# Performance work log

Hardware: AMD Instinct MI355X
Metric: run time of the kernel (lower is better)

Reference implementation:

```python
import jax, jax.numpy as jnp
import numpy as np

NUM_QUBITS = 21
NUM_LAYERS = 4
ACTION_DIM = 18
STATE_DIM = 2 ** NUM_QUBITS  # amplitude register size


def _rx(t):
    c = jnp.cos(t / 2)
    s = jnp.sin(t / 2)
    return jnp.stack([jnp.stack([c + 0j, -1j * s]), jnp.stack([-1j * s, c + 0j])]).astype(jnp.complex64)


def _ry(t):
    c = jnp.cos(t / 2)
    s = jnp.sin(t / 2)
    return jnp.stack([jnp.stack([c, -s]), jnp.stack([s, c])]).astype(jnp.complex64)


def _rz(t):
    e = jnp.exp(-1j * t / 2).astype(jnp.complex64)
    z = jnp.zeros_like(e)
    return jnp.stack([jnp.stack([e, z]), jnp.stack([z, jnp.conj(e)])])


def apply_1q(psi, U, q):
    # wire 0 is the most-significant bit (PennyLane convention)
    s = psi.reshape(2 ** q, 2, -1)
    s = jnp.einsum('ab,xbz->xaz', U, s)
    return s.reshape(-1)


def apply_cnot(psi, c, t):
    a, b = (c, t) if c < t else (t, c)
    s = psi.reshape(2 ** a, 2, 2 ** (b - a - 1), 2, -1)
    ctrl_ax = 1 if c < t else 3
    tgt_ax = 3 if c < t else 1
    s0 = jax.lax.index_in_dim(s, 0, axis=ctrl_ax, keepdims=False)
    s1 = jax.lax.index_in_dim(s, 1, axis=ctrl_ax, keepdims=False)
    tgt_in_slab = tgt_ax if tgt_ax < ctrl_ax else tgt_ax - 1
    s1 = jnp.flip(s1, axis=tgt_in_slab)  # X on target where control==1
    s = jnp.stack([s0, s1], axis=ctrl_ax)
    return s.reshape(-1)


def _layer(psi, lp, entangle):
    # lp: (NUM_QUBITS, 3) rotation angles for this layer
    for q in range(NUM_QUBITS):
        psi = apply_1q(psi, _rx(lp[q, 0]), q)
        psi = apply_1q(psi, _ry(lp[q, 1]), q)
        psi = apply_1q(psi, _rz(lp[q, 2]), q)
    if entangle:
        for q in range(NUM_QUBITS - 1):
            psi = apply_cnot(psi, q, q + 1)
        psi = apply_cnot(psi, NUM_QUBITS - 1, 0)
    return psi


def setup_inputs() -> dict:
    key = jax.random.key(0)
    k1, k2, k3, k4 = jax.random.split(key, 4)
    state = jax.random.normal(k1, (STATE_DIM,), dtype=jnp.float32)
    circuit_params = jax.random.normal(k2, (NUM_LAYERS * NUM_QUBITS * 3,), dtype=jnp.float32) * 0.01
    bound = 1.0 / np.sqrt(NUM_QUBITS)
    head_w = jax.random.uniform(k3, (ACTION_DIM, NUM_QUBITS), jnp.float32, -bound, bound)
    head_b = jax.random.uniform(k4, (ACTION_DIM,), jnp.float32, -bound, bound)
    return {'state': state, 'circuit_params': circuit_params, 'head_w': head_w, 'head_b': head_b}


def reference(state, circuit_params, head_w, head_b):
    # Amplitude encoding: normalize (state_dim == 2**num_qubits so no padding needed)
    norm = jnp.linalg.norm(state)
    inv = jnp.where(norm > 0, 1.0 / jnp.maximum(norm, 1e-30), 0.0)
    basis0 = jnp.zeros((STATE_DIM,), jnp.float32).at[0].set(1.0)
    amp = jnp.where(norm > 0, state * inv, basis0)
    psi = amp.astype(jnp.complex64)

    lp = circuit_params.reshape(NUM_LAYERS, NUM_QUBITS, 3)
    for layer in range(NUM_LAYERS):
        psi = _layer(psi, lp[layer], layer < NUM_LAYERS - 1)

    # Pauli-Z expectation values per qubit from |psi|^2
    probs = psi.real ** 2 + psi.imag ** 2
    zvals = []
    for q in range(NUM_QUBITS):
        p = probs.reshape(2 ** q, 2, -1)
        zvals.append(p[:, 0, :].sum() - p[:, 1, :].sum())
    meas = jnp.stack(zvals).astype(jnp.float32)

    logits = head_w @ meas + head_b
    return jax.nn.softmax(logits, axis=-1)
```

## Files before the change

### kernel.cpp

```cpp
#include <hip/hip_runtime.h>

#define NQ 21
#define DIM (1 << NQ)
#define NL 4
#define ADIM 18

__device__ __forceinline__ float2 cmul(float2 a, float2 b) {
    return make_float2(a.x * b.x - a.y * b.y, a.x * b.y + a.y * b.x);
}
__device__ __forceinline__ float2 cfma2(float2 u0, float2 a, float2 u1, float2 b) {
    return make_float2(u0.x * a.x - u0.y * a.y + u1.x * b.x - u1.y * b.y,
                       u0.x * a.y + u0.y * a.x + u1.x * b.y + u1.y * b.x);
}

__device__ __forceinline__ int pxor8(int x) {
    x ^= x >> 1; x ^= x >> 2; x ^= x >> 4;
    return x & 0xFF;
}

__global__ void k_mats(const float* __restrict__ p, float2* __restrict__ mats) {
    int g = blockIdx.x * blockDim.x + threadIdx.x;
    if (g >= NL * NQ) return;
    const float* ang = p + g * 3;
    float a = ang[0], b = ang[1], c = ang[2];
    float ca = cosf(0.5f * a), sa = sinf(0.5f * a);
    float cb = cosf(0.5f * b), sb = sinf(0.5f * b);
    float cc = cosf(0.5f * c), sc = sinf(0.5f * c);
    float2 m00 = make_float2(cb * ca,  sb * sa);
    float2 m01 = make_float2(-sb * ca, -cb * sa);
    float2 m10 = make_float2(sb * ca,  -cb * sa);
    float2 m11 = make_float2(cb * ca,  -sb * sa);
    float2 ph0 = make_float2(cc, -sc);
    float2 ph1 = make_float2(cc,  sc);
    mats[g * 4 + 0] = cmul(ph0, m00);
    mats[g * 4 + 1] = cmul(ph0, m01);
    mats[g * 4 + 2] = cmul(ph1, m10);
    mats[g * 4 + 3] = cmul(ph1, m11);
}

__global__ __launch_bounds__(512) void k_passA(float2* __restrict__ psi, const float2* __restrict__ mats,
                                               int layer, int entangle, float* __restrict__ partials) {
    __shared__ float4 lds4[4096];
    float2* lds = (float2*)lds4;
    const int blk = blockIdx.x, tid = threadIdx.x;

    const float4* g4 = (const float4*)psi + blk * 4096;
    for (int i = tid; i < 4096; i += 512) lds4[i] = g4[i];
    __syncthreads();

    for (int k = 0; k < 13; ++k) {
        const float2* U = mats + (layer * NQ + (20 - k)) * 4;
        float2 u00 = U[0], u01 = U[1], u10 = U[2], u11 = U[3];
        int m = 1 << k;
        for (int p = tid; p < 4096; p += 512) {
            int i0 = ((p >> k) << (k + 1)) | (p & (m - 1));
            int i1 = i0 | m;
            float2 a = lds[i0], b = lds[i1];
            lds[i0] = cfma2(u00, a, u01, b);
            lds[i1] = cfma2(u10, a, u11, b);
        }
        __syncthreads();
    }

    if (partials) {
        float tot = 0.f;
        float ones[NQ];
#pragma unroll
        for (int q = 0; q < NQ; ++q) ones[q] = 0.f;
        for (int t = tid; t < 8192; t += 512) {
            float2 a = lds[t];
            float pr = a.x * a.x + a.y * a.y;
            int gidx = (blk << 13) | t;
            tot += pr;
#pragma unroll
            for (int q = 0; q < NQ; ++q)
                ones[q] += ((gidx >> (20 - q)) & 1) ? pr : 0.f;
        }
        for (int off = 32; off; off >>= 1) {
            tot += __shfl_down(tot, off, 64);
#pragma unroll
            for (int q = 0; q < NQ; ++q) ones[q] += __shfl_down(ones[q], off, 64);
        }
        __syncthreads();
        float* red = (float*)lds4;
        int wave = tid >> 6, lane = tid & 63;
        if (lane == 0) {
            red[wave * 22 + 21] = tot;
#pragma unroll
            for (int q = 0; q < NQ; ++q) red[wave * 22 + q] = ones[q];
        }
        __syncthreads();
        if (tid < 22) {
            float s = 0.f;
            for (int w = 0; w < 8; ++w) s += red[w * 22 + tid];
            partials[blk * 22 + tid] = s;
        }
    } else if (entangle) {
        float4* o4 = (float4*)psi + blk * 4096;
        int cbit = (blk & 1) << 12;
        for (int t = tid; t < 4096; t += 512) {
            int j0 = 2 * t, j1 = j0 + 1;
            int s0 = (j0 ^ ((j0 >> 1) & 0xFFF)) ^ cbit;
            int s1 = (j1 ^ ((j1 >> 1) & 0xFFF)) ^ cbit;
            float2 e0 = lds[s0], e1 = lds[s1];
            o4[t] = make_float4(e0.x, e0.y, e1.x, e1.y);
        }
    } else {
        float4* o4 = (float4*)psi + blk * 4096;
        for (int t = tid; t < 4096; t += 512) o4[t] = lds4[t];
    }
}

__global__ __launch_bounds__(512) void k_passB(const float* __restrict__ state, float2* __restrict__ psi,
                                               const float2* __restrict__ mats, int layer, int c4, int c1) {
    __shared__ float2 lds[8192];
    const int blk = blockIdx.x, tid = threadIdx.x;

    if (state) {
        const float4* s4 = (const float4*)state;
        for (int t = tid; t < 2048; t += 512) {
            int hs = t >> 3, c = t & 7;
            float4 v = s4[(hs << 11) | (blk << 3) | c];
            int base = hs * 32 + 4 * c;
            lds[base + 0] = make_float2(v.x, 0.f);
            lds[base + 1] = make_float2(v.y, 0.f);
            lds[base + 2] = make_float2(v.z, 0.f);
            lds[base + 3] = make_float2(v.w, 0.f);
        }
    } else {
        const float4* p4 = (const float4*)psi;
        for (int t = tid; t < 4096; t += 512) {
            int hs = t >> 4, c = t & 15;
            float4 v = p4[(hs << 12) | (blk << 4) | c];
            int hodd = c4 ? (hs ^ 128) : hs;
            lds[hs * 32 + 2 * c]       = make_float2(v.x, v.y);
            lds[hodd * 32 + 2 * c + 1] = make_float2(v.z, v.w);
        }
    }
    __syncthreads();

    for (int kb = 0; kb < 8; ++kb) {
        const float2* U = mats + (layer * NQ + (7 - kb)) * 4;
        float2 u00 = U[0], u01 = U[1], u10 = U[2], u11 = U[3];
        for (int p = tid; p < 4096; p += 512) {
            int l = p & 31, hp = p >> 5;
            int h0 = ((hp >> kb) << (kb + 1)) | (hp & ((1 << kb) - 1));
            int i0 = h0 * 32 + l;
            int i1 = i0 + (32 << kb);
            float2 a = lds[i0], b = lds[i1];
            lds[i0] = cfma2(u00, a, u01, b);
            lds[i1] = cfma2(u10, a, u11, b);
        }
        __syncthreads();
    }

    float4* o4 = (float4*)psi;
    for (int t = tid; t < 4096; t += 512) {
        int hs = t >> 4, c = t & 15;
        int hd = c1 ? pxor8(hs) : hs;
        float2 e0 = lds[hs * 32 + 2 * c], e1 = lds[hs * 32 + 2 * c + 1];
        o4[(hd << 12) | (blk << 4) | c] = make_float4(e0.x, e0.y, e1.x, e1.y);
    }
}

__global__ void k_final(const float* __restrict__ partials, const float* __restrict__ head_w,
                        const float* __restrict__ head_b, float* __restrict__ out) {
    __shared__ float red[22];
    __shared__ float meas[NQ];
    __shared__ float lg[ADIM];
    int tid = threadIdx.x;
    if (tid < 22) {
        float s = 0.f;
        for (int b = 0; b < 256; ++b) s += partials[b * 22 + tid];
        red[tid] = s;
    }
    __syncthreads();
    if (tid < NQ) {
        float tot = red[21];
        meas[tid] = (tot > 0.f) ? (1.f - 2.f * red[tid] / tot) : 1.f;
    }
    __syncthreads();
    if (tid < ADIM) {
        float s = head_b[tid];
        for (int q = 0; q < NQ; ++q) s += head_w[tid * NQ + q] * meas[q];
        lg[tid] = s;
    }
    __syncthreads();
    if (tid == 0) {
        float m = lg[0];
        for (int a = 1; a < ADIM; ++a) m = fmaxf(m, lg[a]);
        float s = 0.f;
        for (int a = 0; a < ADIM; ++a) s += expf(lg[a] - m);
        float inv = 1.f / s;
        for (int a = 0; a < ADIM; ++a) out[a] = expf(lg[a] - m) * inv;
    }
}

extern "C" void kernel_launch(void* const* d_in, const int* in_sizes, int n_in,
                              void* d_out, int out_size, void* d_ws, size_t ws_size,
                              hipStream_t stream) {
    const float* state   = (const float*)d_in[0];
    const float* cparams = (const float*)d_in[1];
    const float* head_w  = (const float*)d_in[2];
    const float* head_b  = (const float*)d_in[3];
    float* out = (float*)d_out;

    char* ws = (char*)d_ws;
    float2* psi      = (float2*)ws;
    float2* mats     = (float2*)(ws + (size_t)DIM * 8);
    float*  partials = (float*)(ws + (size_t)DIM * 8 + 4096);

    k_mats<<<1, 128, 0, stream>>>(cparams, mats);
    k_passB<<<256, 512, 0, stream>>>(state,   psi, mats, 0, 0, 1);
    k_passA<<<256, 512, 0, stream>>>(psi, mats, 0, 1, nullptr);
    k_passB<<<256, 512, 0, stream>>>(nullptr, psi, mats, 1, 1, 1);
    k_passA<<<256, 512, 0, stream>>>(psi, mats, 1, 1, nullptr);
    k_passB<<<256, 512, 0, stream>>>(nullptr, psi, mats, 2, 1, 1);
    k_passA<<<256, 512, 0, stream>>>(psi, mats, 2, 1, nullptr);
    k_passB<<<256, 512, 0, stream>>>(nullptr, psi, mats, 3, 1, 0);
    k_passA<<<256, 512, 0, stream>>>(psi, mats, 3, 0, partials);

    k_final<<<1, 64, 0, stream>>>(partials, head_w, head_b, out);
}
```

Baseline: 233.9 us.

## Fuse all circuit passes into one persistent kernel with grid-wide barriers

Replaces the ten separate kernel launches (matrix setup, alternating pass A/B per layer, final reduction) with a single persistent kernel of 512 blocks. Blocks synchronise through an atomic-counter grid barrier, and gate matrices are computed per block in shared memory. The tiles are smaller (4096 amplitudes), and some gates are applied in registers right after the global loads. The aim is to remove launch gaps and tail effects between passes. In exchange it relies on all 512 blocks being co-resident, adds spin-wait barrier overhead, and needs a memset per call.

```diff
diff --git a/kernel.cpp b/kernel.cpp
--- a/kernel.cpp
+++ b/kernel.cpp
@@ -4,195 +4,252 @@
 #define DIM (1 << NQ)
 #define NL 4
 #define ADIM 18
-
-__device__ __forceinline__ float2 cmul(float2 a, float2 b) {
-    return make_float2(a.x * b.x - a.y * b.y, a.x * b.y + a.y * b.x);
-}
+#define GB 512
+#define NT 512
+
 __device__ __forceinline__ float2 cfma2(float2 u0, float2 a, float2 u1, float2 b) {
     return make_float2(u0.x * a.x - u0.y * a.y + u1.x * b.x - u1.y * b.y,
                        u0.x * a.y + u0.y * a.x + u1.x * b.y + u1.y * b.x);
 }
 
-__device__ __forceinline__ int pxor8(int x) {
-    x ^= x >> 1; x ^= x >> 2; x ^= x >> 4;
-    return x & 0xFF;
-}
-
-__global__ void k_mats(const float* __restrict__ p, float2* __restrict__ mats) {
-    int g = blockIdx.x * blockDim.x + threadIdx.x;
-    if (g >= NL * NQ) return;
-    const float* ang = p + g * 3;
-    float a = ang[0], b = ang[1], c = ang[2];
-    float ca = cosf(0.5f * a), sa = sinf(0.5f * a);
-    float cb = cosf(0.5f * b), sb = sinf(0.5f * b);
-    float cc = cosf(0.5f * c), sc = sinf(0.5f * c);
-    float2 m00 = make_float2(cb * ca,  sb * sa);
-    float2 m01 = make_float2(-sb * ca, -cb * sa);
-    float2 m10 = make_float2(sb * ca,  -cb * sa);
-    float2 m11 = make_float2(cb * ca,  -sb * sa);
-    float2 ph0 = make_float2(cc, -sc);
-    float2 ph1 = make_float2(cc,  sc);
-    mats[g * 4 + 0] = cmul(ph0, m00);
-    mats[g * 4 + 1] = cmul(ph0, m01);
-    mats[g * 4 + 2] = cmul(ph1, m10);
-    mats[g * 4 + 3] = cmul(ph1, m11);
-}
-
-__global__ __launch_bounds__(512) void k_passA(float2* __restrict__ psi, const float2* __restrict__ mats,
-                                               int layer, int entangle, float* __restrict__ partials) {
-    __shared__ float4 lds4[4096];
-    float2* lds = (float2*)lds4;
-    const int blk = blockIdx.x, tid = threadIdx.x;
-
-    const float4* g4 = (const float4*)psi + blk * 4096;
-    for (int i = tid; i < 4096; i += 512) lds4[i] = g4[i];
+struct GateU { float2 u00, u01, u10, u11; };
+
+__device__ __forceinline__ void bfly(float2& a, float2& b, const GateU& U) {
+    float2 na = cfma2(U.u00, a, U.u01, b);
+    float2 nb = cfma2(U.u10, a, U.u11, b);
+    a = na; b = nb;
+}
+
+__device__ __forceinline__ void gbar(int* bar, int phase) {
     __syncthreads();
-
-    for (int k = 0; k < 13; ++k) {
-        const float2* U = mats + (layer * NQ + (20 - k)) * 4;
-        float2 u00 = U[0], u01 = U[1], u10 = U[2], u11 = U[3];
-        int m = 1 << k;
-        for (int p = tid; p < 4096; p += 512) {
-            int i0 = ((p >> k) << (k + 1)) | (p & (m - 1));
-            int i1 = i0 | m;
-            float2 a = lds[i0], b = lds[i1];
-            lds[i0] = cfma2(u00, a, u01, b);
-            lds[i1] = cfma2(u10, a, u11, b);
-        }
-        __syncthreads();
-    }
-
-    if (partials) {
-        float tot = 0.f;
-        float ones[NQ];
-#pragma unroll
-        for (int q = 0; q < NQ; ++q) ones[q] = 0.f;
-        for (int t = tid; t < 8192; t += 512) {
-            float2 a = lds[t];
-            float pr = a.x * a.x + a.y * a.y;
-            int gidx = (blk << 13) | t;
-            tot += pr;
-#pragma unroll
-            for (int q = 0; q < NQ; ++q)
-                ones[q] += ((gidx >> (20 - q)) & 1) ? pr : 0.f;
-        }
-        for (int off = 32; off; off >>= 1) {
-            tot += __shfl_down(tot, off, 64);
-#pragma unroll
-            for (int q = 0; q < NQ; ++q) ones[q] += __shfl_down(ones[q], off, 64);
-        }
-        __syncthreads();
-        float* red = (float*)lds4;
-        int wave = tid >> 6, lane = tid & 63;
-        if (lane == 0) {
-            red[wave * 22 + 21] = tot;
-#pragma unroll
-            for (int q = 0; q < NQ; ++q) red[wave * 22 + q] = ones[q];
-        }
-        __syncthreads();
-        if (tid < 22) {
-            float s = 0.f;
-            for (int w = 0; w < 8; ++w) s += red[w * 22 + tid];
-            partials[blk * 22 + tid] = s;
-        }
-    } else if (entangle) {
-        float4* o4 = (float4*)psi + blk * 4096;
-        int cbit = (blk & 1) << 12;
-        for (int t = tid; t < 4096; t += 512) {
-            int j0 = 2 * t, j1 = j0 + 1;
-            int s0 = (j0 ^ ((j0 >> 1) & 0xFFF)) ^ cbit;
-            int s1 = (j1 ^ ((j1 >> 1) & 0xFFF)) ^ cbit;
-            float2 e0 = lds[s0], e1 = lds[s1];
-            o4[t] = make_float4(e0.x, e0.y, e1.x, e1.y);
-        }
-    } else {
-        float4* o4 = (float4*)psi + blk * 4096;
-        for (int t = tid; t < 4096; t += 512) o4[t] = lds4[t];
-    }
-}
-
-__global__ __launch_bounds__(512) void k_passB(const float* __restrict__ state, float2* __restrict__ psi,
-                                               const float2* __restrict__ mats, int layer, int c4, int c1) {
-    __shared__ float2 lds[8192];
-    const int blk = blockIdx.x, tid = threadIdx.x;
-
-    if (state) {
-        const float4* s4 = (const float4*)state;
-        for (int t = tid; t < 2048; t += 512) {
-            int hs = t >> 3, c = t & 7;
-            float4 v = s4[(hs << 11) | (blk << 3) | c];
-            int base = hs * 32 + 4 * c;
-            lds[base + 0] = make_float2(v.x, 0.f);
-            lds[base + 1] = make_float2(v.y, 0.f);
-            lds[base + 2] = make_float2(v.z, 0.f);
-            lds[base + 3] = make_float2(v.w, 0.f);
-        }
-    } else {
-        const float4* p4 = (const float4*)psi;
-        for (int t = tid; t < 4096; t += 512) {
-            int hs = t >> 4, c = t & 15;
-            float4 v = p4[(hs << 12) | (blk << 4) | c];
-            int hodd = c4 ? (hs ^ 128) : hs;
-            lds[hs * 32 + 2 * c]       = make_float2(v.x, v.y);
-            lds[hodd * 32 + 2 * c + 1] = make_float2(v.z, v.w);
-        }
+    if (threadIdx.x == 0) {
+        __threadfence();
+        atomicAdd(bar, 1);
+        const int target = (phase + 1) * GB;
+        while (atomicAdd(bar, 0) < target) __builtin_amdgcn_s_sleep(4);
+        __threadfence();
     }
     __syncthreads();
-
-    for (int kb = 0; kb < 8; ++kb) {
-        const float2* U = mats + (layer * NQ + (7 - kb)) * 4;
-        float2 u00 = U[0], u01 = U[1], u10 = U[2], u11 = U[3];
-        for (int p = tid; p < 4096; p += 512) {
-            int l = p & 31, hp = p >> 5;
-            int h0 = ((hp >> kb) << (kb + 1)) | (hp & ((1 << kb) - 1));
-            int i0 = h0 * 32 + l;
-            int i1 = i0 + (32 << kb);
-            float2 a = lds[i0], b = lds[i1];
-            lds[i0] = cfma2(u00, a, u01, b);
-            lds[i1] = cfma2(u10, a, u11, b);
-        }
-        __syncthreads();
-    }
-
-    float4* o4 = (float4*)psi;
-    for (int t = tid; t < 4096; t += 512) {
-        int hs = t >> 4, c = t & 15;
-        int hd = c1 ? pxor8(hs) : hs;
-        float2 e0 = lds[hs * 32 + 2 * c], e1 = lds[hs * 32 + 2 * c + 1];
-        o4[(hd << 12) | (blk << 4) | c] = make_float4(e0.x, e0.y, e1.x, e1.y);
-    }
-}
-
-__global__ void k_final(const float* __restrict__ partials, const float* __restrict__ head_w,
-                        const float* __restrict__ head_b, float* __restrict__ out) {
-    __shared__ float red[22];
+}
+
+__global__ __launch_bounds__(NT, 4) void qpn_kernel(
+    const float* __restrict__ state, const float* __restrict__ cp,
+    const float* __restrict__ head_w, const float* __restrict__ head_b,
+    float* __restrict__ out, float2* __restrict__ psi, float* __restrict__ partials,
+    int* __restrict__ bar)
+{
+    __shared__ float2 tile[4096];
+    __shared__ GateU mats[NL * NQ];
     __shared__ float meas[NQ];
     __shared__ float lg[ADIM];
-    int tid = threadIdx.x;
-    if (tid < 22) {
-        float s = 0.f;
-        for (int b = 0; b < 256; ++b) s += partials[b * 22 + tid];
-        red[tid] = s;
+    const int tid = threadIdx.x;
+    const int blk = blockIdx.x;
+    float4* psi4 = (float4*)psi;
+    float4* t4 = (float4*)tile;
+    int phase = 0;
+
+    if (tid < NL * NQ) {
+        float a = cp[tid * 3 + 0], b = cp[tid * 3 + 1], c = cp[tid * 3 + 2];
+        float ca = cosf(0.5f * a), sa = sinf(0.5f * a);
+        float cb = cosf(0.5f * b), sb = sinf(0.5f * b);
+        float cc = cosf(0.5f * c), sc = sinf(0.5f * c);
+        float2 m00 = make_float2(cb * ca,  sb * sa);
+        float2 m01 = make_float2(-sb * ca, -cb * sa);
+        float2 m10 = make_float2(sb * ca,  -cb * sa);
+        float2 m11 = make_float2(cb * ca,  -sb * sa);
+        GateU U;
+        U.u00 = make_float2(cc * m00.x + sc * m00.y, cc * m00.y - sc * m00.x);
+        U.u01 = make_float2(cc * m01.x + sc * m01.y, cc * m01.y - sc * m01.x);
+        U.u10 = make_float2(cc * m10.x - sc * m10.y, cc * m10.y + sc * m10.x);
+        U.u11 = make_float2(cc * m11.x - sc * m11.y, cc * m11.y + sc * m11.x);
+        mats[tid] = U;
     }
     __syncthreads();
-    if (tid < NQ) {
-        float tot = red[21];
-        meas[tid] = (tot > 0.f) ? (1.f - 2.f * red[tid] / tot) : 1.f;
-    }
-    __syncthreads();
-    if (tid < ADIM) {
-        float s = head_b[tid];
-        for (int q = 0; q < NQ; ++q) s += head_w[tid * NQ + q] * meas[q];
-        lg[tid] = s;
-    }
-    __syncthreads();
-    if (tid == 0) {
-        float m = lg[0];
-        for (int a = 1; a < ADIM; ++a) m = fmaxf(m, lg[a]);
-        float s = 0.f;
-        for (int a = 0; a < ADIM; ++a) s += expf(lg[a] - m);
-        float inv = 1.f / s;
-        for (int a = 0; a < ADIM; ++a) out[a] = expf(lg[a] - m) * inv;
+
+    for (int layer = 0; layer < NL; ++layer) {
+        if (layer == 0) {
+            const float4* s4 = (const float4*)state;
+            for (int it = 0; it < 2; ++it) {
+                int f2 = it * NT + tid;
+                int h = f2 >> 1, c2 = f2 & 1;
+                float4 w = s4[(h << 10) | (blk << 1) | c2];
+                t4[h * 4 + 2 * c2]     = make_float4(w.x, 0.f, w.y, 0.f);
+                t4[h * 4 + 2 * c2 + 1] = make_float4(w.z, 0.f, w.w, 0.f);
+            }
+            __syncthreads();
+            for (int kb = 0; kb <= 8; ++kb) {
+                GateU U = mats[layer * NQ + (8 - kb)];
+                for (int it = 0; it < 4; ++it) {
+                    int p = it * NT + tid;
+                    int l = p & 7, hp = p >> 3;
+                    int h0 = ((hp >> kb) << (kb + 1)) | (hp & ((1 << kb) - 1));
+                    int i0 = h0 * 8 + l;
+                    bfly(tile[i0], tile[i0 + (8 << kb)], U);
+                }
+                __syncthreads();
+            }
+        } else {
+            float2 v[8];
+            float4 w[4];
+            for (int i = 0; i < 4; ++i) {
+                int f = i * NT + tid;
+                int h = f >> 2, c = f & 3;
+                w[i] = psi4[(h << 11) | (blk << 2) | c];
+            }
+#pragma unroll
+            for (int i = 0; i < 4; ++i) {
+                v[2 * i]     = make_float2(w[i].x, w[i].y);
+                v[2 * i + 1] = make_float2(w[i ^ 2].z, w[i ^ 2].w);
+            }
+            {
+                GateU U0 = mats[layer * NQ + 0];
+#pragma unroll
+                for (int s = 0; s < 8; ++s) if (!(s & 4)) bfly(v[s], v[s | 4], U0);
+                GateU U1 = mats[layer * NQ + 1];
+#pragma unroll
+                for (int s = 0; s < 8; ++s) if (!(s & 2)) bfly(v[s], v[s | 2], U1);
+            }
+            for (int i = 0; i < 4; ++i)
+                t4[i * NT + tid] = make_float4(v[2 * i].x, v[2 * i].y, v[2 * i + 1].x, v[2 * i + 1].y);
+            __syncthreads();
+            for (int kb = 0; kb <= 6; ++kb) {
+                GateU U = mats[layer * NQ + (8 - kb)];
+                for (int it = 0; it < 4; ++it) {
+                    int p = it * NT + tid;
+                    int l = p & 7, hp = p >> 3;
+                    int h0 = ((hp >> kb) << (kb + 1)) | (hp & ((1 << kb) - 1));
+                    int i0 = h0 * 8 + l;
+                    bfly(tile[i0], tile[i0 + (8 << kb)], U);
+                }
+                __syncthreads();
+            }
+        }
+        {
+            int srcmask = (layer < 3) ? 0xFF : 0;
+            for (int i = 0; i < 4; ++i) {
+                int f = i * NT + tid;
+                int h = f >> 2, c = f & 3;
+                int hs = h ^ ((h >> 1) & srcmask);
+                float2 e0 = tile[hs * 8 + 2 * c], e1 = tile[hs * 8 + 2 * c + 1];
+                psi4[(h << 11) | (blk << 2) | c] = make_float4(e0.x, e0.y, e1.x, e1.y);
+            }
+        }
+        gbar(bar, phase++);
+
+        {
+            const float4* ga = psi4 + (size_t)blk * 2048;
+            float2 v[8];
+            float4 w[4];
+            for (int i = 0; i < 4; ++i) w[i] = ga[i * NT + tid];
+#pragma unroll
+            for (int i = 0; i < 4; ++i) {
+                v[2 * i]     = make_float2(w[i].x, w[i].y);
+                v[2 * i + 1] = make_float2(w[i].z, w[i].w);
+            }
+            GateU U20 = mats[layer * NQ + 20];
+#pragma unroll
+            for (int s = 0; s < 8; s += 2) bfly(v[s], v[s + 1], U20);
+            GateU U10 = mats[layer * NQ + 10];
+#pragma unroll
+            for (int s = 0; s < 8; ++s) if (!(s & 2)) bfly(v[s], v[s | 2], U10);
+            GateU U9 = mats[layer * NQ + 9];
+#pragma unroll
+            for (int s = 0; s < 8; ++s) if (!(s & 4)) bfly(v[s], v[s | 4], U9);
+            for (int i = 0; i < 4; ++i)
+                t4[i * NT + tid] = make_float4(v[2 * i].x, v[2 * i].y, v[2 * i + 1].x, v[2 * i + 1].y);
+        }
+        __syncthreads();
+        for (int k = 1; k <= 9; ++k) {
+            GateU U = mats[layer * NQ + (20 - k)];
+            int m = 1 << k;
+            for (int it = 0; it < 4; ++it) {
+                int p = it * NT + tid;
+                int i0 = ((p >> k) << (k + 1)) | (p & (m - 1));
+                bfly(tile[i0], tile[i0 | m], U);
+            }
+            __syncthreads();
+        }
+        if (layer < 3) {
+            float4* oa = psi4 + (size_t)blk * 2048;
+            int cb = (blk & 1) << 11;
+            for (int i = 0; i < 4; ++i) {
+                int f = i * NT + tid;
+                int s0 = ((2 * f) ^ (f & 0x7FF)) ^ cb;
+                float2 e0 = tile[s0], e1 = tile[s0 ^ 1];
+                oa[f] = make_float4(e0.x, e0.y, e1.x, e1.y);
+            }
+            gbar(bar, phase++);
+        } else {
+            float tot = 0.f, ones[NQ];
+#pragma unroll
+            for (int q = 0; q < NQ; ++q) ones[q] = 0.f;
+            for (int it = 0; it < 8; ++it) {
+                int j = it * NT + tid;
+                float2 a2 = tile[j];
+                float pr = a2.x * a2.x + a2.y * a2.y;
+                int gidx = (blk << 12) | j;
+                tot += pr;
+#pragma unroll
+                for (int q = 0; q < NQ; ++q)
+                    ones[q] += pr * (float)((gidx >> (20 - q)) & 1);
+            }
+            for (int off = 32; off; off >>= 1) {
+                tot += __shfl_down(tot, off, 64);
+#pragma unroll
+                for (int q = 0; q < NQ; ++q) ones[q] += __shfl_down(ones[q], off, 64);
+            }
+            __syncthreads();
+            float* red = (float*)tile;
+            int wv = tid >> 6, ln = tid & 63;
+            if (ln == 0) {
+                red[wv * 22 + 21] = tot;
+#pragma unroll
+                for (int q = 0; q < NQ; ++q) red[wv * 22 + q] = ones[q];
+            }
+            __syncthreads();
+            if (tid < 22) {
+                float s = 0.f;
+                for (int wvi = 0; wvi < 8; ++wvi) s += red[wvi * 22 + tid];
+                partials[blk * 22 + tid] = s;
+            }
+            gbar(bar, phase++);
+        }
+    }
+
+    if (blk == 0) {
+        float* red = (float*)tile;
+        int col = tid % 22, grp = tid / 22;
+        if (tid < 506) {
+            float s = 0.f;
+            for (int r = grp; r < GB; r += 23) s += partials[r * 22 + col];
+            red[grp * 22 + col] = s;
+        }
+        __syncthreads();
+        if (tid < 22) {
+            float t2 = 0.f;
+            for (int g = 0; g < 23; ++g) t2 += red[g * 22 + tid];
+            red[600 + tid] = t2;
+        }
+        __syncthreads();
+        if (tid < NQ) {
+            float tot = red[600 + 21];
+            meas[tid] = (tot > 0.f) ? (1.f - 2.f * red[600 + tid] / tot) : 1.f;
+        }
+        __syncthreads();
+        if (tid < ADIM) {
+            float s2 = head_b[tid];
+            for (int q = 0; q < NQ; ++q) s2 += head_w[tid * NQ + q] * meas[q];
+            lg[tid] = s2;
+        }
+        __syncthreads();
+        if (tid == 0) {
+            float m = lg[0];
+            for (int a = 1; a < ADIM; ++a) m = fmaxf(m, lg[a]);
+            float ssum = 0.f;
+            for (int a = 0; a < ADIM; ++a) ssum += expf(lg[a] - m);
+            float inv = 1.f / ssum;
+            for (int a = 0; a < ADIM; ++a) out[a] = expf(lg[a] - m) * inv;
+        }
     }
 }
 
@@ -205,20 +262,10 @@
     const float* head_b  = (const float*)d_in[3];
     float* out = (float*)d_out;
 
-    char* ws = (char*)d_ws;
-    float2* psi      = (float2*)ws;
-    float2* mats     = (float2*)(ws + (size_t)DIM * 8);
-    float*  partials = (float*)(ws + (size_t)DIM * 8 + 4096);
-
-    k_mats<<<1, 128, 0, stream>>>(cparams, mats);
-    k_passB<<<256, 512, 0, stream>>>(state,   psi, mats, 0, 0, 1);
-    k_passA<<<256, 512, 0, stream>>>(psi, mats, 0, 1, nullptr);
-    k_passB<<<256, 512, 0, stream>>>(nullptr, psi, mats, 1, 1, 1);
-    k_passA<<<256, 512, 0, stream>>>(psi, mats, 1, 1, nullptr);
-    k_passB<<<256, 512, 0, stream>>>(nullptr, psi, mats, 2, 1, 1);
-    k_passA<<<256, 512, 0, stream>>>(psi, mats, 2, 1, nullptr);
-    k_passB<<<256, 512, 0, stream>>>(nullptr, psi, mats, 3, 1, 0);
-    k_passA<<<256, 512, 0, stream>>>(psi, mats, 3, 0, partials);
-
-    k_final<<<1, 64, 0, stream>>>(partials, head_w, head_b, out);
-}
+    float2* psi      = (float2*)d_ws;
+    float*  partials = (float*)((char*)d_ws + (size_t)DIM * 8);
+    int*    bar      = (int*)((char*)d_ws + (size_t)DIM * 8 + 65536);
+
+    hipMemsetAsync(bar, 0, 64, stream);
+    qpn_kernel<<<GB, NT, 0, stream>>>(state, cparams, head_w, head_b, out, psi, partials, bar);
+}
```

Result: slower. 748.2 us (+219.9%).
